# Kernel tuning notes

Hardware: AMD Instinct MI355X
Metric: run time of the kernel (lower is better)

## Reference

```python
import jax, jax.numpy as jnp
import numpy as np

N_HEADS = 4


def setup_inputs() -> dict:
    key = jax.random.key(0)
    k1, k2, k3 = jax.random.split(key, 3)
    B, C, H, W = 2, 128, 64, 64
    x = jax.random.normal(k1, (B, C, H, W), dtype=jnp.float32)
    w_qkv = jax.random.normal(k2, (3 * C, C), dtype=jnp.float32) * (1.0 / np.sqrt(C))
    b_qkv = jnp.zeros((3 * C,), dtype=jnp.float32)
    w_proj = jax.random.normal(k3, (C, C), dtype=jnp.float32) * (1.0 / np.sqrt(C))
    b_proj = jnp.zeros((C,), dtype=jnp.float32)
    return {"x": x, "w_qkv": w_qkv, "b_qkv": b_qkv, "w_proj": w_proj, "b_proj": b_proj}


def reference(x, w_qkv, b_qkv, w_proj, b_proj):
    B, C, H, W = x.shape
    nh = N_HEADS
    ch = C // nh  # per-head channels
    T = H * W
    # 1x1 conv qkv projection: (B, 3C, H, W)
    qkv = jnp.einsum('bchw,oc->bohw', x, w_qkv) + b_qkv[None, :, None, None]
    # split into heads: (B*nh, 3*ch, T) -> q, k, v each (B*nh, ch, T)
    qkv = qkv.reshape(B * nh, 3 * ch, T)
    q, k, v = qkv[:, :ch], qkv[:, ch:2 * ch], qkv[:, 2 * ch:]
    scale = jnp.asarray(1.0 / np.sqrt(np.sqrt(ch)), dtype=x.dtype)
    # attention weights over flattened spatial tokens: (B*nh, T, T)
    weight = jnp.einsum('bct,bcs->bts', q * scale, k * scale)
    weight = jax.nn.softmax(weight, axis=-1)  # stable softmax == max-subtracted softmax
    a = jnp.einsum('bts,bcs->bct', weight, v)  # (B*nh, ch, T)
    a = a.reshape(B, C, H, W)
    # 1x1 conv output projection + residual
    h = jnp.einsum('bchw,oc->bohw', a, w_proj) + b_proj[None, :, None, None]
    return x + h
```

## Files before the change

kernel.cpp:

```cpp
#include <hip/hip_runtime.h>


typedef _Float16 f16;
typedef _Float16 f16x8 __attribute__((ext_vector_type(8)));
typedef _Float16 f16x4 __attribute__((ext_vector_type(4)));
typedef float    f32x4 __attribute__((ext_vector_type(4)));

#define T_DIM 4096
#define C_DIM 128
#define CH    32
#define NH    4
#define NBH   8
#define SPLITS 8
#define S_SPLIT (T_DIM / SPLITS)
#define NTILES  (S_SPLIT / 64)
#define FIXED_M 8.0f

__global__ __launch_bounds__(256) void k_qkv2(const float* __restrict__ x,
                                              const float* __restrict__ wqkv,
                                              const float* __restrict__ bqkv,
                                              f16* __restrict__ qh,
                                              f16* __restrict__ kh,
                                              f16* __restrict__ vt) {
  __shared__ f16 Xs[64][C_DIM + 8];
  int tid = threadIdx.x;
  int w = tid >> 6, lane = tid & 63;
  int l15 = lane & 15, quad = lane >> 4;
  int o0 = blockIdx.x * 64 + w * 16;
  int t0 = blockIdx.y * 64;
  int b  = blockIdx.z;

  {
    int tl = tid & 63, cg = tid >> 6;
    const float* xb = x + (size_t)b * C_DIM * T_DIM;
#pragma unroll 4
    for (int k = 0; k < 32; k += 2) {
      int c = cg * 32 + k;
      float v0 = xb[(size_t)c * T_DIM + t0 + tl];
      float v1 = xb[(size_t)(c + 1) * T_DIM + t0 + tl];
      unsigned p = __builtin_bit_cast(unsigned, __builtin_amdgcn_cvt_pkrtz(v0, v1));
      *(unsigned*)&Xs[tl][c] = p;
    }
  }
  __syncthreads();

  f32x4 acc[4] = {{0,0,0,0},{0,0,0,0},{0,0,0,0},{0,0,0,0}};
#pragma unroll
  for (int kc = 0; kc < 4; ++kc) {
    const float* wp = wqkv + (size_t)(o0 + l15) * C_DIM + kc * 32 + quad * 8;
    f16x8 af;
#pragma unroll
    for (int i = 0; i < 8; ++i) af[i] = (f16)wp[i];
#pragma unroll
    for (int nf = 0; nf < 4; ++nf) {
      f16x8 bf = *(const f16x8*)&Xs[nf * 16 + l15][kc * 32 + quad * 8];
      acc[nf] = __builtin_amdgcn_mfma_f32_16x16x32_f16(af, bf, acc[nf], 0, 0, 0);
    }
  }
  int ob   = o0 + quad * 4;
  int head = ob / 96;
  int r96  = ob % 96;
  int grp  = r96 >> 5;
  int c0   = r96 & 31;
  int bh   = b * NH + head;
  float bias[4];
#pragma unroll
  for (int r = 0; r < 4; ++r) bias[r] = bqkv[ob + r];
  const float SCALE2 = 0.17677669529663687f * 1.4426950408889634f;
#pragma unroll
  for (int nf = 0; nf < 4; ++nf) {
    int t = t0 + nf * 16 + l15;
    float v[4];
#pragma unroll
    for (int r = 0; r < 4; ++r) v[r] = acc[nf][r] + bias[r];
    if (grp == 0) {
      f16x4 q;
#pragma unroll
      for (int r = 0; r < 4; ++r) q[r] = (f16)(v[r] * SCALE2);
      *(f16x4*)(qh + ((size_t)bh * T_DIM + t) * CH + c0) = q;
    } else if (grp == 1) {
      f16x4 kk;
#pragma unroll
      for (int r = 0; r < 4; ++r) kk[r] = (f16)v[r];
      *(f16x4*)(kh + ((size_t)bh * T_DIM + t) * CH + c0) = kk;
    } else {
#pragma unroll
      for (int r = 0; r < 4; ++r)
        vt[((size_t)bh * CH + c0 + r) * T_DIM + t] = (f16)v[r];
    }
  }
}

__global__ __launch_bounds__(256, 4) void k_attn(const f16* __restrict__ qh,
                                                 const f16* __restrict__ kh,
                                                 const f16* __restrict__ vt,
                                                 f16* __restrict__ outp,
                                                 float* __restrict__ ml) {
  __shared__ f16 Ks[64][40];
  __shared__ f16 Vs[32][72];
  __shared__ f16 Ps[4][32][72];
  int tid = threadIdx.x;
  int w = tid >> 6, lane = tid & 63;
  int l15 = lane & 15, quad = lane >> 4;
  int combo = blockIdx.x;
  int bh    = combo & 7;
  int split = combo >> 3;
  int q0    = blockIdx.y * 128 + w * 32;
  int s_base = split * S_SPLIT;

  f16x8 qf[2];
#pragma unroll
  for (int nq = 0; nq < 2; ++nq)
    qf[nq] = *(const f16x8*)(qh + ((size_t)bh * T_DIM + q0 + nq * 16 + l15) * CH + quad * 8);

  f32x4 acc[2][2] = {{{0,0,0,0},{0,0,0,0}},{{0,0,0,0},{0,0,0,0}}};
  float llane[2] = {0.f, 0.f};
  const f32x4 zf = {0.f, 0.f, 0.f, 0.f};

  const f16* kbase = kh + ((size_t)bh * T_DIM + s_base + (tid >> 2)) * CH + (tid & 3) * 8;
  const f16* vbase = vt + ((size_t)bh * CH + (tid >> 3)) * T_DIM + s_base + (tid & 7) * 8;
  f16* ksdst = &Ks[tid >> 2][(tid & 3) * 8];
  f16* vsdst = &Vs[tid >> 3][(tid & 7) * 8];

#pragma unroll 1
  for (int tile = 0; tile < NTILES; ++tile) {
    __syncthreads();
    *(uint4*)ksdst = *(const uint4*)kbase;
    *(uint4*)vsdst = *(const uint4*)vbase;
    kbase += 64 * CH;
    vbase += 64;
    __syncthreads();

    {
      f16x8 kf[4];
#pragma unroll
      for (int nf = 0; nf < 4; ++nf)
        kf[nf] = *(const f16x8*)&Ks[nf * 16 + l15][quad * 8];
#pragma unroll
      for (int nq = 0; nq < 2; ++nq) {
        f32x4 st[4];
#pragma unroll
        for (int nf = 0; nf < 4; ++nf)
          st[nf] = __builtin_amdgcn_mfma_f32_16x16x32_f16(kf[nf], qf[nq], zf, 0, 0, 0);
#pragma unroll
        for (int nf = 0; nf < 4; ++nf) {
          float e0 = __builtin_amdgcn_exp2f(st[nf][0] - FIXED_M);
          float e1 = __builtin_amdgcn_exp2f(st[nf][1] - FIXED_M);
          float e2 = __builtin_amdgcn_exp2f(st[nf][2] - FIXED_M);
          float e3 = __builtin_amdgcn_exp2f(st[nf][3] - FIXED_M);
          llane[nq] += (e0 + e1) + (e2 + e3);
          uint2 pk;
          pk.x = __builtin_bit_cast(unsigned, __builtin_amdgcn_cvt_pkrtz(e0, e1));
          pk.y = __builtin_bit_cast(unsigned, __builtin_amdgcn_cvt_pkrtz(e2, e3));
          *(uint2*)&Ps[w][nq * 16 + l15][nf * 16 + quad * 4] = pk;
        }
      }
    }

#pragma unroll
    for (int kc = 0; kc < 2; ++kc) {
      f16x8 vf0 = *(const f16x8*)&Vs[l15][kc * 32 + quad * 8];
      f16x8 vf1 = *(const f16x8*)&Vs[16 + l15][kc * 32 + quad * 8];
#pragma unroll
      for (int nq = 0; nq < 2; ++nq) {
        f16x8 pf = *(const f16x8*)&Ps[w][nq * 16 + l15][kc * 32 + quad * 8];
        acc[0][nq] = __builtin_amdgcn_mfma_f32_16x16x32_f16(vf0, pf, acc[0][nq], 0, 0, 0);
        acc[1][nq] = __builtin_amdgcn_mfma_f32_16x16x32_f16(vf1, pf, acc[1][nq], 0, 0, 0);
      }
    }
  }

#pragma unroll
  for (int nq = 0; nq < 2; ++nq) {
    float l = llane[nq];
    l += __shfl_xor(l, 16);
    l += __shfl_xor(l, 32);
    int q = q0 + nq * 16 + l15;
    size_t base = ((size_t)(split * NBH + bh) * T_DIM + q) * CH;
#pragma unroll
    for (int cs = 0; cs < 2; ++cs) {
      uint2 h;
      h.x = __builtin_bit_cast(unsigned, __builtin_amdgcn_cvt_pkrtz(acc[cs][nq][0], acc[cs][nq][1]));
      h.y = __builtin_bit_cast(unsigned, __builtin_amdgcn_cvt_pkrtz(acc[cs][nq][2], acc[cs][nq][3]));
      *(uint2*)(outp + base + cs * 16 + quad * 4) = h;
    }
    if (quad == 0)
      ml[(size_t)(split * NBH + bh) * T_DIM + q] = l;
  }
}

__global__ __launch_bounds__(256) void k_proj2(const f16* __restrict__ outp,
                                               const float* __restrict__ ml,
                                               const float* __restrict__ wp,
                                               const float* __restrict__ bp,
                                               const float* __restrict__ x,
                                               float* __restrict__ out) {
  __shared__ float Lt[NH][32];
  __shared__ f16 Ahs[32][C_DIM + 8];
  int tid = threadIdx.x;
  int b  = blockIdx.y;
  int t0 = blockIdx.x * 32;

  if (tid < 128) {
    int head = tid >> 5, t = tid & 31;
    float L = 0.f;
#pragma unroll
    for (int s = 0; s < SPLITS; ++s)
      L += ml[(size_t)(s * NBH + b * NH + head) * T_DIM + t0 + t];
    Lt[head][t] = L;
  }
  __syncthreads();

  {
    int t = tid >> 3, cg = tid & 7;
    int head = cg >> 1, c0 = cg * 16;
    float o[16];
#pragma unroll
    for (int i = 0; i < 16; ++i) o[i] = 0.f;
#pragma unroll
    for (int s = 0; s < SPLITS; ++s) {
      const f16* p = outp + ((size_t)(s * NBH + b * NH + head) * T_DIM + t0 + t) * CH + (cg & 1) * 16;
      f16x8 v0 = *(const f16x8*)p;
      f16x8 v1 = *(const f16x8*)(p + 8);
#pragma unroll
      for (int i = 0; i < 8; ++i) { o[i] += (float)v0[i]; o[8 + i] += (float)v1[i]; }
    }
    float inv = 1.0f / Lt[head][t];
    f16x8 h0, h1;
#pragma unroll
    for (int i = 0; i < 8; ++i) { h0[i] = (f16)(o[i] * inv); h1[i] = (f16)(o[8 + i] * inv); }
    *(f16x8*)&Ahs[t][c0]     = h0;
    *(f16x8*)&Ahs[t][c0 + 8] = h1;
  }
  __syncthreads();

  int w = tid >> 6, lane = tid & 63;
  int l15 = lane & 15, quad = lane >> 4;
  int o0 = w * 32;
  f32x4 acc[2][2] = {{{0,0,0,0},{0,0,0,0}},{{0,0,0,0},{0,0,0,0}}};
#pragma unroll
  for (int kc = 0; kc < 4; ++kc) {
    f16x8 af[2];
#pragma unroll
    for (int os = 0; os < 2; ++os) {
      const float* wr = wp + (size_t)(o0 + os * 16 + l15) * C_DIM + kc * 32 + quad * 8;
#pragma unroll
      for (int i = 0; i < 8; ++i) af[os][i] = (f16)wr[i];
    }
#pragma unroll
    for (int ts = 0; ts < 2; ++ts) {
      f16x8 bf = *(const f16x8*)&Ahs[ts * 16 + l15][kc * 32 + quad * 8];
#pragma unroll
      for (int os = 0; os < 2; ++os)
        acc[os][ts] = __builtin_amdgcn_mfma_f32_16x16x32_f16(af[os], bf, acc[os][ts], 0, 0, 0);
    }
  }
#pragma unroll
  for (int os = 0; os < 2; ++os) {
    int ob = o0 + os * 16 + quad * 4;
    float bias[4];
#pragma unroll
    for (int r = 0; r < 4; ++r) bias[r] = bp[ob + r];
#pragma unroll
    for (int ts = 0; ts < 2; ++ts) {
#pragma unroll
      for (int r = 0; r < 4; ++r) {
        int t = t0 + ts * 16 + l15;
        size_t idx = ((size_t)(b * C_DIM) + ob + r) * T_DIM + t;
        out[idx] = x[idx] + bias[r] + acc[os][ts][r];
      }
    }
  }
}

extern "C" void kernel_launch(void* const* d_in, const int* in_sizes, int n_in,
                              void* d_out, int out_size, void* d_ws, size_t ws_size,
                              hipStream_t stream) {
  const float* x     = (const float*)d_in[0];
  const float* wqkv  = (const float*)d_in[1];
  const float* bqkv  = (const float*)d_in[2];
  const float* wproj = (const float*)d_in[3];
  const float* bproj = (const float*)d_in[4];
  float* out = (float*)d_out;

  char* ws = (char*)d_ws;
  f16*   Qh   = (f16*)(ws);
  f16*   Kh   = (f16*)(ws + (2u << 20));
  f16*   Vt   = (f16*)(ws + (4u << 20));
  f16*   OutP = (f16*)(ws + (6u << 20));
  float* ML   = (float*)(ws + (22u << 20));

  k_qkv2<<<dim3(6, 64, 2), 256, 0, stream>>>(x, wqkv, bqkv, Qh, Kh, Vt);
  k_attn<<<dim3(NBH * SPLITS, T_DIM / 128), 256, 0, stream>>>(Qh, Kh, Vt, OutP, ML);
  k_proj2<<<dim3(T_DIM / 32, 2), 256, 0, stream>>>(OutP, ML, wproj, bproj, x, out);
}
```

Baseline: 114.4 us.

## Pre-convert weights to fp16 and retile QKV/proj kernels to 16-token blocks

Adds a small kernel that converts the QKV and output-projection weights to fp16 once per call. The QKV kernel now processes 16 tokens per block, with each wave computing all 96 outputs of one head, so x is read once per token tile instead of six times across output tiles. The projection kernel also moves to 16-token blocks and loads fp16 weights directly. The intent is to remove redundant fp32 weight loads and per-element conversions and to reduce repeated x traffic, at the cost of an extra launch and smaller tiles with less weight reuse per block.

Measured after the change: 116.9 us. 2.3% more time.

```diff
diff --git a/kernel.cpp b/kernel.cpp
--- a/kernel.cpp
+++ b/kernel.cpp
@@ -16,63 +16,73 @@
 #define NTILES  (S_SPLIT / 64)
 #define FIXED_M 8.0f
 
-__global__ __launch_bounds__(256) void k_qkv2(const float* __restrict__ x,
-                                              const float* __restrict__ wqkv,
+__global__ __launch_bounds__(256) void k_wcvt(const float* __restrict__ wqkv,
+                                              const float* __restrict__ wproj,
+                                              f16* __restrict__ whq,
+                                              f16* __restrict__ whp) {
+  int idx = (blockIdx.x * 256 + threadIdx.x) * 4;
+  const int NQ = 384 * C_DIM;
+  const float* src;
+  f16* dst;
+  int j;
+  if (idx < NQ) { src = wqkv; dst = whq; j = idx; }
+  else          { src = wproj; dst = whp; j = idx - NQ; }
+  float4 v = *(const float4*)(src + j);
+  f16x4 h;
+  h[0] = (f16)v.x; h[1] = (f16)v.y; h[2] = (f16)v.z; h[3] = (f16)v.w;
+  *(f16x4*)(dst + j) = h;
+}
+
+__global__ __launch_bounds__(256) void k_qkv3(const float* __restrict__ x,
+                                              const f16* __restrict__ whq,
                                               const float* __restrict__ bqkv,
                                               f16* __restrict__ qh,
                                               f16* __restrict__ kh,
                                               f16* __restrict__ vt) {
-  __shared__ f16 Xs[64][C_DIM + 8];
+  __shared__ f16 Xs[16][C_DIM + 8];
   int tid = threadIdx.x;
   int w = tid >> 6, lane = tid & 63;
   int l15 = lane & 15, quad = lane >> 4;
-  int o0 = blockIdx.x * 64 + w * 16;
-  int t0 = blockIdx.y * 64;
-  int b  = blockIdx.z;
+  int t0 = blockIdx.x * 16;
+  int b  = blockIdx.y;
 
   {
-    int tl = tid & 63, cg = tid >> 6;
+    int tl = tid & 15, cg = tid >> 4;
     const float* xb = x + (size_t)b * C_DIM * T_DIM;
-#pragma unroll 4
-    for (int k = 0; k < 32; k += 2) {
-      int c = cg * 32 + k;
+#pragma unroll
+    for (int k = 0; k < 8; k += 2) {
+      int c = cg * 8 + k;
       float v0 = xb[(size_t)c * T_DIM + t0 + tl];
       float v1 = xb[(size_t)(c + 1) * T_DIM + t0 + tl];
-      unsigned p = __builtin_bit_cast(unsigned, __builtin_amdgcn_cvt_pkrtz(v0, v1));
-      *(unsigned*)&Xs[tl][c] = p;
+      *(unsigned*)&Xs[tl][c] =
+          __builtin_bit_cast(unsigned, __builtin_amdgcn_cvt_pkrtz(v0, v1));
     }
   }
   __syncthreads();
 
-  f32x4 acc[4] = {{0,0,0,0},{0,0,0,0},{0,0,0,0},{0,0,0,0}};
+  f32x4 acc[6] = {{0,0,0,0},{0,0,0,0},{0,0,0,0},{0,0,0,0},{0,0,0,0},{0,0,0,0}};
 #pragma unroll
   for (int kc = 0; kc < 4; ++kc) {
-    const float* wp = wqkv + (size_t)(o0 + l15) * C_DIM + kc * 32 + quad * 8;
-    f16x8 af;
-#pragma unroll
-    for (int i = 0; i < 8; ++i) af[i] = (f16)wp[i];
-#pragma unroll
-    for (int nf = 0; nf < 4; ++nf) {
-      f16x8 bf = *(const f16x8*)&Xs[nf * 16 + l15][kc * 32 + quad * 8];
-      acc[nf] = __builtin_amdgcn_mfma_f32_16x16x32_f16(af, bf, acc[nf], 0, 0, 0);
-    }
-  }
-  int ob   = o0 + quad * 4;
-  int head = ob / 96;
-  int r96  = ob % 96;
-  int grp  = r96 >> 5;
-  int c0   = r96 & 31;
-  int bh   = b * NH + head;
-  float bias[4];
-#pragma unroll
-  for (int r = 0; r < 4; ++r) bias[r] = bqkv[ob + r];
+    f16x8 bf = *(const f16x8*)&Xs[l15][kc * 32 + quad * 8];
+#pragma unroll
+    for (int os = 0; os < 6; ++os) {
+      f16x8 af = *(const f16x8*)(whq + (size_t)(w * 96 + os * 16 + l15) * C_DIM + kc * 32 + quad * 8);
+      acc[os] = __builtin_amdgcn_mfma_f32_16x16x32_f16(af, bf, acc[os], 0, 0, 0);
+    }
+  }
+
+  int bh = b * NH + w;
+  int t  = t0 + l15;
   const float SCALE2 = 0.17677669529663687f * 1.4426950408889634f;
 #pragma unroll
-  for (int nf = 0; nf < 4; ++nf) {
-    int t = t0 + nf * 16 + l15;
+  for (int os = 0; os < 6; ++os) {
+    int r96 = os * 16 + quad * 4;
+    int grp = r96 >> 5;
+    int c0  = r96 & 31;
+    int o   = w * 96 + r96;
     float v[4];
 #pragma unroll
-    for (int r = 0; r < 4; ++r) v[r] = acc[nf][r] + bias[r];
+    for (int r = 0; r < 4; ++r) v[r] = acc[os][r] + bqkv[o + r];
     if (grp == 0) {
       f16x4 q;
 #pragma unroll
@@ -189,20 +199,20 @@
   }
 }
 
-__global__ __launch_bounds__(256) void k_proj2(const f16* __restrict__ outp,
+__global__ __launch_bounds__(256) void k_proj3(const f16* __restrict__ outp,
                                                const float* __restrict__ ml,
-                                               const float* __restrict__ wp,
+                                               const f16* __restrict__ whp,
                                                const float* __restrict__ bp,
                                                const float* __restrict__ x,
                                                float* __restrict__ out) {
-  __shared__ float Lt[NH][32];
-  __shared__ f16 Ahs[32][C_DIM + 8];
+  __shared__ float Lt[NH][16];
+  __shared__ f16 Ahs[16][C_DIM + 8];
   int tid = threadIdx.x;
   int b  = blockIdx.y;
-  int t0 = blockIdx.x * 32;
-
-  if (tid < 128) {
-    int head = tid >> 5, t = tid & 31;
+  int t0 = blockIdx.x * 16;
+
+  if (tid < 64) {
+    int head = tid >> 4, t = tid & 15;
     float L = 0.f;
 #pragma unroll
     for (int s = 0; s < SPLITS; ++s)
@@ -212,47 +222,35 @@
   __syncthreads();
 
   {
-    int t = tid >> 3, cg = tid & 7;
-    int head = cg >> 1, c0 = cg * 16;
-    float o[16];
-#pragma unroll
-    for (int i = 0; i < 16; ++i) o[i] = 0.f;
+    int t = tid >> 4, cg = tid & 15;
+    int head = cg >> 2, c0 = (cg & 3) * 8;
+    float o[8] = {0.f, 0.f, 0.f, 0.f, 0.f, 0.f, 0.f, 0.f};
 #pragma unroll
     for (int s = 0; s < SPLITS; ++s) {
-      const f16* p = outp + ((size_t)(s * NBH + b * NH + head) * T_DIM + t0 + t) * CH + (cg & 1) * 16;
-      f16x8 v0 = *(const f16x8*)p;
-      f16x8 v1 = *(const f16x8*)(p + 8);
-#pragma unroll
-      for (int i = 0; i < 8; ++i) { o[i] += (float)v0[i]; o[8 + i] += (float)v1[i]; }
+      f16x8 v = *(const f16x8*)(outp +
+          ((size_t)(s * NBH + b * NH + head) * T_DIM + t0 + t) * CH + c0);
+#pragma unroll
+      for (int i = 0; i < 8; ++i) o[i] += (float)v[i];
     }
     float inv = 1.0f / Lt[head][t];
-    f16x8 h0, h1;
-#pragma unroll
-    for (int i = 0; i < 8; ++i) { h0[i] = (f16)(o[i] * inv); h1[i] = (f16)(o[8 + i] * inv); }
-    *(f16x8*)&Ahs[t][c0]     = h0;
-    *(f16x8*)&Ahs[t][c0 + 8] = h1;
+    f16x8 h;
+#pragma unroll
+    for (int i = 0; i < 8; ++i) h[i] = (f16)(o[i] * inv);
+    *(f16x8*)&Ahs[t][head * 32 + c0] = h;
   }
   __syncthreads();
 
   int w = tid >> 6, lane = tid & 63;
   int l15 = lane & 15, quad = lane >> 4;
   int o0 = w * 32;
-  f32x4 acc[2][2] = {{{0,0,0,0},{0,0,0,0}},{{0,0,0,0},{0,0,0,0}}};
+  f32x4 acc[2] = {{0,0,0,0},{0,0,0,0}};
 #pragma unroll
   for (int kc = 0; kc < 4; ++kc) {
-    f16x8 af[2];
+    f16x8 bf = *(const f16x8*)&Ahs[l15][kc * 32 + quad * 8];
 #pragma unroll
     for (int os = 0; os < 2; ++os) {
-      const float* wr = wp + (size_t)(o0 + os * 16 + l15) * C_DIM + kc * 32 + quad * 8;
-#pragma unroll
-      for (int i = 0; i < 8; ++i) af[os][i] = (f16)wr[i];
-    }
-#pragma unroll
-    for (int ts = 0; ts < 2; ++ts) {
-      f16x8 bf = *(const f16x8*)&Ahs[ts * 16 + l15][kc * 32 + quad * 8];
-#pragma unroll
-      for (int os = 0; os < 2; ++os)
-        acc[os][ts] = __builtin_amdgcn_mfma_f32_16x16x32_f16(af[os], bf, acc[os][ts], 0, 0, 0);
+      f16x8 af = *(const f16x8*)(whp + (size_t)(o0 + os * 16 + l15) * C_DIM + kc * 32 + quad * 8);
+      acc[os] = __builtin_amdgcn_mfma_f32_16x16x32_f16(af, bf, acc[os], 0, 0, 0);
     }
   }
 #pragma unroll
@@ -262,13 +260,10 @@
 #pragma unroll
     for (int r = 0; r < 4; ++r) bias[r] = bp[ob + r];
 #pragma unroll
-    for (int ts = 0; ts < 2; ++ts) {
-#pragma unroll
-      for (int r = 0; r < 4; ++r) {
-        int t = t0 + ts * 16 + l15;
-        size_t idx = ((size_t)(b * C_DIM) + ob + r) * T_DIM + t;
-        out[idx] = x[idx] + bias[r] + acc[os][ts][r];
-      }
+    for (int r = 0; r < 4; ++r) {
+      int t = t0 + l15;
+      size_t idx = ((size_t)(b * C_DIM) + ob + r) * T_DIM + t;
+      out[idx] = x[idx] + bias[r] + acc[os][r];
     }
   }
 }
@@ -284,13 +279,16 @@
   float* out = (float*)d_out;
 
   char* ws = (char*)d_ws;
-  f16*   Qh   = (f16*)(ws);
-  f16*   Kh   = (f16*)(ws + (2u << 20));
-  f16*   Vt   = (f16*)(ws + (4u << 20));
-  f16*   OutP = (f16*)(ws + (6u << 20));
-  float* ML   = (float*)(ws + (22u << 20));
-
-  k_qkv2<<<dim3(6, 64, 2), 256, 0, stream>>>(x, wqkv, bqkv, Qh, Kh, Vt);
+  f16*   Whq  = (f16*)(ws);
+  f16*   Whp  = (f16*)(ws + (1u << 20));
+  f16*   Qh   = (f16*)(ws + (2u << 20));
+  f16*   Kh   = (f16*)(ws + (4u << 20));
+  f16*   Vt   = (f16*)(ws + (6u << 20));
+  f16*   OutP = (f16*)(ws + (8u << 20));
+  float* ML   = (float*)(ws + (24u << 20));
+
+  k_wcvt<<<dim3(64), 256, 0, stream>>>(wqkv, wproj, Whq, Whp);
+  k_qkv3<<<dim3(T_DIM / 16, 2), 256, 0, stream>>>(x, Whq, bqkv, Qh, Kh, Vt);
   k_attn<<<dim3(NBH * SPLITS, T_DIM / 128), 256, 0, stream>>>(Qh, Kh, Vt, OutP, ML);
-  k_proj2<<<dim3(T_DIM / 32, 2), 256, 0, stream>>>(OutP, ML, wproj, bproj, x, out);
-}
+  k_proj3<<<dim3(T_DIM / 16, 2), 256, 0, stream>>>(OutP, ML, Whp, bproj, x, out);
+}
```
